# Optimization experiments

Measured on AMD Instinct MI355X. Metric: run time of the kernel, lower is better.

## Reference

```python
import jax, jax.numpy as jnp
import numpy as np

B, T, E = 64, 512, 128
NODES, PATHS, OUT = 100000, 200000, 1000
PAD = 1  # padding_idx for node embedding


def setup_inputs() -> dict:
    key = jax.random.key(0)
    ks = jax.random.split(key, 10)
    starts = jax.random.randint(ks[0], (B, T), 0, NODES)
    paths = jax.random.randint(ks[1], (B, T), 0, PATHS)
    ends = jax.random.randint(ks[2], (B, T), 0, NODES)
    length = jax.random.randint(ks[3], (B,), 0, T)
    node_emb = jax.random.normal(ks[4], (NODES, E), dtype=jnp.float32)
    path_emb = jax.random.normal(ks[5], (PATHS, E), dtype=jnp.float32)
    W = jax.random.normal(ks[6], (E, 3 * E), dtype=jnp.float32)
    a = jax.random.normal(ks[7], (E,), dtype=jnp.float32)
    out_W = jax.random.normal(ks[8], (OUT, E), dtype=jnp.float32) * (1.0 / np.sqrt(E))
    out_b = jax.random.normal(ks[9], (OUT,), dtype=jnp.float32) * 0.01
    return dict(starts=starts, paths=paths, ends=ends, length=length,
                node_emb=node_emb, path_emb=path_emb, W=W, a=a,
                out_W=out_W, out_b=out_b)


def reference(starts, paths, ends, length, node_emb, path_emb, W, a, out_W, out_b):
    # padding_idx=1 -> that embedding row is zero
    node_emb = node_emb.at[PAD].set(0.0)
    es = node_emb[starts]          # [B,T,E]
    ep = path_emb[paths]           # [B,T,E]
    ee = node_emb[ends]            # [B,T,E]
    c = jnp.concatenate([es, ep, ee], axis=2)          # [B,T,3E]
    # dropout is identity in eval mode
    x = jnp.tanh(jnp.einsum('ed,btd->bte', W, c))      # [B,T,E]
    z = jax.nn.softmax(x @ a, axis=1)                  # [B,T] softmax over full T
    # original code sums only first length[i] attention weights (no renorm)
    mask = (jnp.arange(T)[None, :] < length[:, None]).astype(x.dtype)  # [B,T]
    v = jnp.einsum('bte,bt->be', x, z * mask)          # [B,E]
    return v @ out_W.T + out_b                          # [B,OUT]
```

## Files before the change

### kernel.cpp

```cpp
#include <hip/hip_runtime.h>

#define BB     64
#define TT     512
#define EE     128
#define NROWS  (BB * TT)
#define PADIDX 1
#define OUTN   1000

typedef __attribute__((ext_vector_type(8)))  short short8;
typedef __attribute__((ext_vector_type(16))) float f32x16;

__device__ __forceinline__ float tanh_fast(float v) {
    return 1.0f - 2.0f / (__expf(2.0f * v) + 1.0f);
}

__device__ __forceinline__ unsigned short f2bf(float f) {
    unsigned int u = __float_as_uint(f);
    u += 0x7fffu + ((u >> 16) & 1u);
    return (unsigned short)(u >> 16);
}
__device__ __forceinline__ float bf2f(unsigned short h) {
    return __uint_as_float(((unsigned int)h) << 16);
}

__global__ __launch_bounds__(256, 1)
void k_gemm_x(const int* __restrict__ starts, const int* __restrict__ paths,
              const int* __restrict__ ends,
              const float* __restrict__ node_emb, const float* __restrict__ path_emb,
              const float* __restrict__ W, const float* __restrict__ a,
              float* __restrict__ x, float* __restrict__ s)
{
    __shared__ __align__(16) unsigned short Ah[128 * 64];
    __shared__ __align__(16) unsigned short Al[128 * 64];
    __shared__ __align__(16) unsigned short Wh[128 * 64];
    __shared__ __align__(16) unsigned short Wl[128 * 64];
    __shared__ int   idx_lds[3][128];
    __shared__ float s_red[128][2];

    const int tid = threadIdx.x;
    const int r0  = blockIdx.x * 128;

    if (tid < 128) {
        idx_lds[0][tid] = starts[r0 + tid];
        idx_lds[1][tid] = paths [r0 + tid];
        idx_lds[2][tid] = ends  [r0 + tid];
    }

    const int q    = tid & 15;
    const int ty   = tid >> 4;
    const int lane = tid & 63;
    const int wid  = tid >> 6;
    const int wm   = wid >> 1;
    const int wn   = wid & 1;
    const int fr   = lane & 31;
    const int fkb  = (lane >> 5) * 16;

    f32x16 acc[2][2];
#pragma unroll
    for (int mi = 0; mi < 2; ++mi)
#pragma unroll
        for (int ni = 0; ni < 2; ++ni)
#pragma unroll
            for (int i = 0; i < 16; ++i) acc[mi][ni][i] = 0.0f;

    float4 va[8], vw[8];

    __syncthreads();

#define LOAD_STAGE(T) do {                                                      \
    const int seg_ = (T) >> 1;                                                  \
    const int off_ = ((T) & 1) * 64;                                            \
    const float* emb_ = (seg_ == 1) ? path_emb : node_emb;                      \
    const bool isn_ = (seg_ != 1);                                              \
    _Pragma("unroll")                                                           \
    for (int it = 0; it < 8; ++it) {                                            \
        const int row_ = it * 16 + ty;                                          \
        const int idx_ = idx_lds[seg_][row_];                                   \
        va[it] = *((const float4*)(emb_ + (size_t)idx_ * EE + off_) + q);       \
        if (isn_ && idx_ == PADIDX) { va[it].x = 0.f; va[it].y = 0.f;           \
                                      va[it].z = 0.f; va[it].w = 0.f; }         \
        vw[it] = *((const float4*)(W + row_ * 384 + (T) * 64) + q);             \
    }                                                                           \
} while (0)

#define CVT_WRITE() do {                                                        \
    _Pragma("unroll")                                                           \
    for (int it = 0; it < 8; ++it) {                                            \
        const int row_  = it * 16 + ty;                                         \
        const int boff_ = row_ * 128 + ((q * 8) ^ ((row_ & 7) << 4));           \
        {                                                                       \
            const unsigned short h0 = f2bf(va[it].x), h1 = f2bf(va[it].y);      \
            const unsigned short h2 = f2bf(va[it].z), h3 = f2bf(va[it].w);      \
            uint2 hp; hp.x = (unsigned)h0 | ((unsigned)h1 << 16);               \
                      hp.y = (unsigned)h2 | ((unsigned)h3 << 16);               \
            *(uint2*)((char*)Ah + boff_) = hp;                                  \
            const unsigned short l0 = f2bf(va[it].x - bf2f(h0));                \
            const unsigned short l1 = f2bf(va[it].y - bf2f(h1));                \
            const unsigned short l2 = f2bf(va[it].z - bf2f(h2));                \
            const unsigned short l3 = f2bf(va[it].w - bf2f(h3));                \
            uint2 lp; lp.x = (unsigned)l0 | ((unsigned)l1 << 16);               \
                      lp.y = (unsigned)l2 | ((unsigned)l3 << 16);               \
            *(uint2*)((char*)Al + boff_) = lp;                                  \
        }                                                                       \
        {                                                                       \
            const unsigned short h0 = f2bf(vw[it].x), h1 = f2bf(vw[it].y);      \
            const unsigned short h2 = f2bf(vw[it].z), h3 = f2bf(vw[it].w);      \
            uint2 hp; hp.x = (unsigned)h0 | ((unsigned)h1 << 16);               \
                      hp.y = (unsigned)h2 | ((unsigned)h3 << 16);               \
            *(uint2*)((char*)Wh + boff_) = hp;                                  \
            const unsigned short l0 = f2bf(vw[it].x - bf2f(h0));                \
            const unsigned short l1 = f2bf(vw[it].y - bf2f(h1));                \
            const unsigned short l2 = f2bf(vw[it].z - bf2f(h2));                \
            const unsigned short l3 = f2bf(vw[it].w - bf2f(h3));                \
            uint2 lp; lp.x = (unsigned)l0 | ((unsigned)l1 << 16);               \
                      lp.y = (unsigned)l2 | ((unsigned)l3 << 16);               \
            *(uint2*)((char*)Wl + boff_) = lp;                                  \
        }                                                                       \
    }                                                                           \
} while (0)

#define COMPUTE() do {                                                          \
    _Pragma("unroll")                                                           \
    for (int ksub = 0; ksub < 4; ++ksub) {                                      \
        short8 ah[2], al2[2], bh[2], bl2[2];                                    \
        _Pragma("unroll")                                                       \
        for (int mi = 0; mi < 2; ++mi) {                                        \
            const int row_  = wm * 64 + mi * 32 + fr;                           \
            const int boff_ = row_ * 128 + ((ksub * 32 + fkb) ^ ((row_ & 7) << 4)); \
            ah[mi]  = *(const short8*)((const char*)Ah + boff_);                \
            al2[mi] = *(const short8*)((const char*)Al + boff_);                \
        }                                                                       \
        _Pragma("unroll")                                                       \
        for (int ni = 0; ni < 2; ++ni) {                                        \
            const int row_  = wn * 64 + ni * 32 + fr;                           \
            const int boff_ = row_ * 128 + ((ksub * 32 + fkb) ^ ((row_ & 7) << 4)); \
            bh[ni]  = *(const short8*)((const char*)Wh + boff_);                \
            bl2[ni] = *(const short8*)((const char*)Wl + boff_);                \
        }                                                                       \
        _Pragma("unroll")                                                       \
        for (int mi = 0; mi < 2; ++mi)                                          \
        _Pragma("unroll")                                                       \
        for (int ni = 0; ni < 2; ++ni) {                                        \
            acc[mi][ni] = __builtin_amdgcn_mfma_f32_32x32x16_bf16(ah[mi],  bh[ni],  acc[mi][ni], 0, 0, 0); \
            acc[mi][ni] = __builtin_amdgcn_mfma_f32_32x32x16_bf16(ah[mi],  bl2[ni], acc[mi][ni], 0, 0, 0); \
            acc[mi][ni] = __builtin_amdgcn_mfma_f32_32x32x16_bf16(al2[mi], bh[ni],  acc[mi][ni], 0, 0, 0); \
        }                                                                       \
    }                                                                           \
} while (0)

    LOAD_STAGE(0);
    CVT_WRITE();
    __syncthreads();

    for (int t = 0; t < 6; ++t) {
        if (t < 5) LOAD_STAGE(t + 1);
        COMPUTE();
        __syncthreads();
        if (t < 5) { CVT_WRITE(); __syncthreads(); }
    }

    const float a0 = a[wn * 64 + fr];
    const float a1 = a[wn * 64 + 32 + fr];
    const int hi_half = lane >> 5;

#pragma unroll
    for (int mi = 0; mi < 2; ++mi) {
        float sp[16];
#pragma unroll
        for (int r = 0; r < 16; ++r) sp[r] = 0.0f;
#pragma unroll
        for (int ni = 0; ni < 2; ++ni) {
            const float ac  = (ni == 0) ? a0 : a1;
            const int   col = wn * 64 + ni * 32 + fr;
#pragma unroll
            for (int r = 0; r < 16; ++r) {
                const int rowl = (r & 3) + 8 * (r >> 2) + 4 * hi_half;
                const float tv = tanh_fast(acc[mi][ni][r]);
                x[(size_t)(r0 + wm * 64 + mi * 32 + rowl) * EE + col] = tv;
                sp[r] = fmaf(tv, ac, sp[r]);
            }
        }
#pragma unroll
        for (int m = 1; m < 32; m <<= 1)
#pragma unroll
            for (int r = 0; r < 16; ++r) sp[r] += __shfl_xor(sp[r], m, 64);
        if (fr == 0) {
#pragma unroll
            for (int r = 0; r < 16; ++r) {
                const int rowl = (r & 3) + 8 * (r >> 2) + 4 * hi_half;
                s_red[wm * 64 + mi * 32 + rowl][wn] = sp[r];
            }
        }
    }
    __syncthreads();
    if (tid < 128) s[r0 + tid] = s_red[tid][0] + s_red[tid][1];
}

__global__ __launch_bounds__(256)
void k_attn(const float* __restrict__ s, const int* __restrict__ length,
            const float* __restrict__ x, float* __restrict__ v)
{
    __shared__ float sw[TT];
    __shared__ float red[256];

    const int b   = blockIdx.x >> 2;
    const int ec  = blockIdx.x & 3;
    const int tid = threadIdx.x;

    const float s0 = s[b * TT + tid];
    const float s1 = s[b * TT + 256 + tid];

    red[tid] = fmaxf(s0, s1);
    __syncthreads();
    for (int st = 128; st > 0; st >>= 1) {
        if (tid < st) red[tid] = fmaxf(red[tid], red[tid + st]);
        __syncthreads();
    }
    const float mx = red[0];
    __syncthreads();

    const float e0 = __expf(s0 - mx);
    const float e1 = __expf(s1 - mx);
    red[tid] = e0 + e1;
    __syncthreads();
    for (int st = 128; st > 0; st >>= 1) {
        if (tid < st) red[tid] += red[tid + st];
        __syncthreads();
    }
    const float inv = 1.0f / red[0];
    const int   len = length[b];
    __syncthreads();

    sw[tid]       = (tid < len)       ? e0 * inv : 0.0f;
    sw[tid + 256] = (tid + 256 < len) ? e1 * inv : 0.0f;
    __syncthreads();

    const int e  = ec * 32 + (tid & 31);
    const int tp = tid >> 5;
    const float* xb = x + (size_t)b * TT * EE;
    float acc = 0.0f;
#pragma unroll 8
    for (int t = tp; t < TT; t += 8)
        acc = fmaf(sw[t], xb[(size_t)t * EE + e], acc);

    red[tid] = acc;
    __syncthreads();
    if (tid < 32) {
        float r2 = 0.0f;
#pragma unroll
        for (int k = 0; k < 8; ++k) r2 += red[k * 32 + tid];
        v[b * EE + ec * 32 + tid] = r2;
    }
}

__global__ __launch_bounds__(256)
void k_out(const float* __restrict__ v, const float* __restrict__ out_W,
           const float* __restrict__ out_b, float* __restrict__ out)
{
    const int id = blockIdx.x * 256 + threadIdx.x;
    const int o  = id >> 6;
    const int bb = id & 63;

    const float4* vr = (const float4*)(v + bb * EE);
    const float4* wr = (const float4*)(out_W + o * EE);
    float acc = 0.0f;
#pragma unroll 8
    for (int qq = 0; qq < 32; ++qq) {
        const float4 a4 = vr[qq];
        const float4 b4 = wr[qq];
        acc = fmaf(a4.x, b4.x, acc);
        acc = fmaf(a4.y, b4.y, acc);
        acc = fmaf(a4.z, b4.z, acc);
        acc = fmaf(a4.w, b4.w, acc);
    }
    out[bb * OUTN + o] = acc + out_b[o];
}

extern "C" void kernel_launch(void* const* d_in, const int* in_sizes, int n_in,
                              void* d_out, int out_size, void* d_ws, size_t ws_size,
                              hipStream_t stream)
{
    const int*   starts   = (const int*)d_in[0];
    const int*   paths    = (const int*)d_in[1];
    const int*   ends     = (const int*)d_in[2];
    const int*   length   = (const int*)d_in[3];
    const float* node_emb = (const float*)d_in[4];
    const float* path_emb = (const float*)d_in[5];
    const float* W        = (const float*)d_in[6];
    const float* a        = (const float*)d_in[7];
    const float* out_W    = (const float*)d_in[8];
    const float* out_b    = (const float*)d_in[9];
    float*       out      = (float*)d_out;

    float* x = (float*)d_ws;
    float* s = x + (size_t)NROWS * EE;
    float* v = s + NROWS;

    k_gemm_x<<<NROWS / 128, 256, 0, stream>>>(starts, paths, ends,
                                              node_emb, path_emb, W, a, x, s);
    k_attn<<<BB * 4, 256, 0, stream>>>(s, length, x, v);
    k_out<<<(BB * OUTN) / 256, 256, 0, stream>>>(v, out_W, out_b, out);
}
```

Baseline: 221.0 us.

## Stream gathered rows into LDS asynchronously with double buffering and precomputed split W

Adds a prep kernel that splits W once into swizzled bf16 hi/lo tiles in workspace. The GEMM kernel now copies gathered embedding rows and the W tiles straight into double-buffered LDS with global_load_lds, using manual vmcnt waits so the next stage loads while the current one computes. The fp32-to-bf16 split of activations moves to register time inside compute. This removes per-stage register staging, conversion and extra barriers, but uses about 130KB of LDS, adds one more launch, and relies on hand-written waitcnt ordering.

```diff
diff --git a/kernel.cpp b/kernel.cpp
--- a/kernel.cpp
+++ b/kernel.cpp
@@ -1,4 +1,5 @@
 #include <hip/hip_runtime.h>
+#include <hip/hip_bf16.h>
 
 #define BB     64
 #define TT     512
@@ -14,46 +15,71 @@
     return 1.0f - 2.0f / (__expf(2.0f * v) + 1.0f);
 }
 
-__device__ __forceinline__ unsigned short f2bf(float f) {
-    unsigned int u = __float_as_uint(f);
-    u += 0x7fffu + ((u >> 16) & 1u);
-    return (unsigned short)(u >> 16);
-}
-__device__ __forceinline__ float bf2f(unsigned short h) {
-    return __uint_as_float(((unsigned int)h) << 16);
+__device__ __forceinline__ void split8(float4 a0, float4 a1, short8& hi, short8& lo) {
+    float f[8] = {a0.x, a0.y, a0.z, a0.w, a1.x, a1.y, a1.z, a1.w};
+#pragma unroll
+    for (int i = 0; i < 8; ++i) {
+        unsigned u = __float_as_uint(f[i]);
+        unsigned r = (u + (0x7fffu + ((u >> 16) & 1u))) & 0xffff0000u;
+        hi[i] = (short)(r >> 16);
+        lo[i] = (short)(__float_as_uint(f[i] - __uint_as_float(r)) >> 16);
+    }
+}
+
+__device__ __forceinline__ void gl_lds16(const void* g, void* l) {
+    __builtin_amdgcn_global_load_lds((const __attribute__((address_space(1))) void*)g,
+                                     (__attribute__((address_space(3))) void*)l, 16, 0, 0);
+}
+
+__global__ __launch_bounds__(256)
+void k_prep(const float* __restrict__ W, unsigned short* __restrict__ Whg,
+            unsigned short* __restrict__ Wlg)
+{
+    const int id = blockIdx.x * 256 + threadIdx.x;
+    const int e  = id & 127;
+    const int d  = id >> 7;
+    const float v = W[e * 384 + d];
+    const int t = d >> 6, k = d & 63;
+
+    unsigned u = __float_as_uint(v);
+    unsigned r = (u + (0x7fffu + ((u >> 16) & 1u))) & 0xffff0000u;
+    const unsigned short h = (unsigned short)(r >> 16);
+    const unsigned short l = (unsigned short)(__float_as_uint(v - __uint_as_float(r)) >> 16);
+
+    const int boff = t * 16384 + e * 128 + ((k * 2) ^ ((e & 7) << 4));
+    *(unsigned short*)((char*)Whg + boff) = h;
+    *(unsigned short*)((char*)Wlg + boff) = l;
 }
 
 __global__ __launch_bounds__(256, 1)
 void k_gemm_x(const int* __restrict__ starts, const int* __restrict__ paths,
               const int* __restrict__ ends,
               const float* __restrict__ node_emb, const float* __restrict__ path_emb,
-              const float* __restrict__ W, const float* __restrict__ a,
-              float* __restrict__ x, float* __restrict__ s)
-{
-    __shared__ __align__(16) unsigned short Ah[128 * 64];
-    __shared__ __align__(16) unsigned short Al[128 * 64];
-    __shared__ __align__(16) unsigned short Wh[128 * 64];
-    __shared__ __align__(16) unsigned short Wl[128 * 64];
-    __shared__ int   idx_lds[3][128];
-    __shared__ float s_red[128][2];
+              const unsigned short* __restrict__ Whg, const unsigned short* __restrict__ Wlg,
+              const float* __restrict__ a, float* __restrict__ x, float* __restrict__ s)
+{
+    extern __shared__ char smem[];
+    float*          Af      = (float*)smem;
+    unsigned short* Wh      = (unsigned short*)(smem + 65536);
+    unsigned short* Wl      = (unsigned short*)(smem + 98304);
+    int*            idx_lds = (int*)(smem + 131072);
+    float*          s_red   = (float*)(smem + 132608);
 
     const int tid = threadIdx.x;
     const int r0  = blockIdx.x * 128;
 
     if (tid < 128) {
-        idx_lds[0][tid] = starts[r0 + tid];
-        idx_lds[1][tid] = paths [r0 + tid];
-        idx_lds[2][tid] = ends  [r0 + tid];
-    }
-
-    const int q    = tid & 15;
-    const int ty   = tid >> 4;
+        idx_lds[0 * 128 + tid] = starts[r0 + tid];
+        idx_lds[1 * 128 + tid] = paths [r0 + tid];
+        idx_lds[2 * 128 + tid] = ends  [r0 + tid];
+    }
+
     const int lane = tid & 63;
-    const int wid  = tid >> 6;
-    const int wm   = wid >> 1;
-    const int wn   = wid & 1;
+    const int w    = tid >> 6;
+    const int wm   = w >> 1;
+    const int wn   = w & 1;
     const int fr   = lane & 31;
-    const int fkb  = (lane >> 5) * 16;
+    const int kh   = lane >> 5;
 
     f32x16 acc[2][2];
 #pragma unroll
@@ -63,105 +89,97 @@
 #pragma unroll
             for (int i = 0; i < 16; ++i) acc[mi][ni][i] = 0.0f;
 
-    float4 va[8], vw[8];
-
-    __syncthreads();
-
-#define LOAD_STAGE(T) do {                                                      \
-    const int seg_ = (T) >> 1;                                                  \
-    const int off_ = ((T) & 1) * 64;                                            \
-    const float* emb_ = (seg_ == 1) ? path_emb : node_emb;                      \
-    const bool isn_ = (seg_ != 1);                                              \
+    __syncthreads();
+
+    bool p0[2], p2[2];
+#pragma unroll
+    for (int mi = 0; mi < 2; ++mi) {
+        const int rm = wm * 64 + mi * 32 + fr;
+        p0[mi] = (idx_lds[0 * 128 + rm] == PADIDX);
+        p2[mi] = (idx_lds[2 * 128 + rm] == PADIDX);
+    }
+
+#define ISSUE(T) do {                                                           \
+    const int   seg_  = (T) >> 1;                                               \
+    const char* embc_ = (const char*)((seg_ == 1) ? path_emb : node_emb);       \
+    char*       afb_  = (char*)Af + (((T) & 1) ? 32768 : 0);                    \
     _Pragma("unroll")                                                           \
     for (int it = 0; it < 8; ++it) {                                            \
-        const int row_ = it * 16 + ty;                                          \
-        const int idx_ = idx_lds[seg_][row_];                                   \
-        va[it] = *((const float4*)(emb_ + (size_t)idx_ * EE + off_) + q);       \
-        if (isn_ && idx_ == PADIDX) { va[it].x = 0.f; va[it].y = 0.f;           \
-                                      va[it].z = 0.f; va[it].w = 0.f; }         \
-        vw[it] = *((const float4*)(W + row_ * 384 + (T) * 64) + q);             \
+        const int row_ = w * 32 + it * 4 + (lane >> 4);                         \
+        const int idx_ = idx_lds[seg_ * 128 + row_];                            \
+        const char* src_ = embc_ + (size_t)idx_ * 512 + ((T) & 1) * 256         \
+                         + (((lane & 15) * 16) ^ ((row_ & 7) << 4));            \
+        gl_lds16(src_, afb_ + (w * 32 + it * 4) * 256);                         \
+    }                                                                           \
+    char* whb_ = (char*)Wh + (((T) & 1) ? 16384 : 0);                           \
+    char* wlb_ = (char*)Wl + (((T) & 1) ? 16384 : 0);                           \
+    _Pragma("unroll")                                                           \
+    for (int rr = 0; rr < 4; ++rr) {                                            \
+        const int o_ = rr * 4096 + w * 1024;                                    \
+        gl_lds16((const char*)Whg + (T) * 16384 + o_ + lane * 16, whb_ + o_);   \
+        gl_lds16((const char*)Wlg + (T) * 16384 + o_ + lane * 16, wlb_ + o_);   \
     }                                                                           \
 } while (0)
 
-#define CVT_WRITE() do {                                                        \
-    _Pragma("unroll")                                                           \
-    for (int it = 0; it < 8; ++it) {                                            \
-        const int row_  = it * 16 + ty;                                         \
-        const int boff_ = row_ * 128 + ((q * 8) ^ ((row_ & 7) << 4));           \
-        {                                                                       \
-            const unsigned short h0 = f2bf(va[it].x), h1 = f2bf(va[it].y);      \
-            const unsigned short h2 = f2bf(va[it].z), h3 = f2bf(va[it].w);      \
-            uint2 hp; hp.x = (unsigned)h0 | ((unsigned)h1 << 16);               \
-                      hp.y = (unsigned)h2 | ((unsigned)h3 << 16);               \
-            *(uint2*)((char*)Ah + boff_) = hp;                                  \
-            const unsigned short l0 = f2bf(va[it].x - bf2f(h0));                \
-            const unsigned short l1 = f2bf(va[it].y - bf2f(h1));                \
-            const unsigned short l2 = f2bf(va[it].z - bf2f(h2));                \
-            const unsigned short l3 = f2bf(va[it].w - bf2f(h3));                \
-            uint2 lp; lp.x = (unsigned)l0 | ((unsigned)l1 << 16);               \
-                      lp.y = (unsigned)l2 | ((unsigned)l3 << 16);               \
-            *(uint2*)((char*)Al + boff_) = lp;                                  \
-        }                                                                       \
-        {                                                                       \
-            const unsigned short h0 = f2bf(vw[it].x), h1 = f2bf(vw[it].y);      \
-            const unsigned short h2 = f2bf(vw[it].z), h3 = f2bf(vw[it].w);      \
-            uint2 hp; hp.x = (unsigned)h0 | ((unsigned)h1 << 16);               \
-                      hp.y = (unsigned)h2 | ((unsigned)h3 << 16);               \
-            *(uint2*)((char*)Wh + boff_) = hp;                                  \
-            const unsigned short l0 = f2bf(vw[it].x - bf2f(h0));                \
-            const unsigned short l1 = f2bf(vw[it].y - bf2f(h1));                \
-            const unsigned short l2 = f2bf(vw[it].z - bf2f(h2));                \
-            const unsigned short l3 = f2bf(vw[it].w - bf2f(h3));                \
-            uint2 lp; lp.x = (unsigned)l0 | ((unsigned)l1 << 16);               \
-                      lp.y = (unsigned)l2 | ((unsigned)l3 << 16);               \
-            *(uint2*)((char*)Wl + boff_) = lp;                                  \
-        }                                                                       \
-    }                                                                           \
-} while (0)
-
-#define COMPUTE() do {                                                          \
+#define COMPUTE(T) do {                                                         \
+    const char* afc_ = (const char*)Af + (((T) & 1) ? 32768 : 0);               \
+    const char* whc_ = (const char*)Wh + (((T) & 1) ? 16384 : 0);               \
+    const char* wlc_ = (const char*)Wl + (((T) & 1) ? 16384 : 0);               \
     _Pragma("unroll")                                                           \
     for (int ksub = 0; ksub < 4; ++ksub) {                                      \
-        short8 ah[2], al2[2], bh[2], bl2[2];                                    \
+        short8 ah[2], al[2], bh[2], bl[2];                                      \
         _Pragma("unroll")                                                       \
         for (int mi = 0; mi < 2; ++mi) {                                        \
-            const int row_  = wm * 64 + mi * 32 + fr;                           \
-            const int boff_ = row_ * 128 + ((ksub * 32 + fkb) ^ ((row_ & 7) << 4)); \
-            ah[mi]  = *(const short8*)((const char*)Ah + boff_);                \
-            al2[mi] = *(const short8*)((const char*)Al + boff_);                \
+            const int row_ = wm * 64 + mi * 32 + fr;                            \
+            const int swz_ = (row_ & 7) << 4;                                   \
+            const int k0b_ = ksub * 64 + kh * 32;                               \
+            float4 a0 = *(const float4*)(afc_ + row_ * 256 + (k0b_ ^ swz_));    \
+            float4 a1 = *(const float4*)(afc_ + row_ * 256 + ((k0b_ + 16) ^ swz_)); \
+            const bool pad_ = ((T) < 2) ? p0[mi] : (((T) >= 4) ? p2[mi] : false); \
+            if (pad_) { a0 = make_float4(0.f, 0.f, 0.f, 0.f); a1 = a0; }        \
+            split8(a0, a1, ah[mi], al[mi]);                                     \
         }                                                                       \
         _Pragma("unroll")                                                       \
         for (int ni = 0; ni < 2; ++ni) {                                        \
-            const int row_  = wn * 64 + ni * 32 + fr;                           \
-            const int boff_ = row_ * 128 + ((ksub * 32 + fkb) ^ ((row_ & 7) << 4)); \
-            bh[ni]  = *(const short8*)((const char*)Wh + boff_);                \
-            bl2[ni] = *(const short8*)((const char*)Wl + boff_);                \
+            const int e_ = wn * 64 + ni * 32 + fr;                              \
+            const int bo_ = e_ * 128 + ((ksub * 32 + kh * 16) ^ ((e_ & 7) << 4)); \
+            bh[ni] = *(const short8*)(whc_ + bo_);                              \
+            bl[ni] = *(const short8*)(wlc_ + bo_);                              \
         }                                                                       \
         _Pragma("unroll")                                                       \
         for (int mi = 0; mi < 2; ++mi)                                          \
         _Pragma("unroll")                                                       \
         for (int ni = 0; ni < 2; ++ni) {                                        \
-            acc[mi][ni] = __builtin_amdgcn_mfma_f32_32x32x16_bf16(ah[mi],  bh[ni],  acc[mi][ni], 0, 0, 0); \
-            acc[mi][ni] = __builtin_amdgcn_mfma_f32_32x32x16_bf16(ah[mi],  bl2[ni], acc[mi][ni], 0, 0, 0); \
-            acc[mi][ni] = __builtin_amdgcn_mfma_f32_32x32x16_bf16(al2[mi], bh[ni],  acc[mi][ni], 0, 0, 0); \
+            acc[mi][ni] = __builtin_amdgcn_mfma_f32_32x32x16_bf16(ah[mi], bh[ni], acc[mi][ni], 0, 0, 0); \
+            acc[mi][ni] = __builtin_amdgcn_mfma_f32_32x32x16_bf16(ah[mi], bl[ni], acc[mi][ni], 0, 0, 0); \
+            acc[mi][ni] = __builtin_amdgcn_mfma_f32_32x32x16_bf16(al[mi], bh[ni], acc[mi][ni], 0, 0, 0); \
         }                                                                       \
     }                                                                           \
 } while (0)
 
-    LOAD_STAGE(0);
-    CVT_WRITE();
-    __syncthreads();
-
+    ISSUE(0);
+
+#pragma unroll
     for (int t = 0; t < 6; ++t) {
-        if (t < 5) LOAD_STAGE(t + 1);
-        COMPUTE();
-        __syncthreads();
-        if (t < 5) { CVT_WRITE(); __syncthreads(); }
-    }
-
-    const float a0 = a[wn * 64 + fr];
-    const float a1 = a[wn * 64 + 32 + fr];
-    const int hi_half = lane >> 5;
+        if (t < 5) {
+            ISSUE(t + 1);
+            asm volatile("s_waitcnt vmcnt(16)" ::: "memory");
+        } else {
+            asm volatile("s_waitcnt vmcnt(0)" ::: "memory");
+        }
+        __builtin_amdgcn_s_barrier();
+        __builtin_amdgcn_sched_barrier(0);
+        COMPUTE(t);
+        asm volatile("s_waitcnt lgkmcnt(0)" ::: "memory");
+        __builtin_amdgcn_sched_barrier(0);
+        __builtin_amdgcn_s_barrier();
+    }
+
+#undef ISSUE
+#undef COMPUTE
+
+    const float a0v = a[wn * 64 + fr];
+    const float a1v = a[wn * 64 + 32 + fr];
 
 #pragma unroll
     for (int mi = 0; mi < 2; ++mi) {
@@ -170,11 +188,11 @@
         for (int r = 0; r < 16; ++r) sp[r] = 0.0f;
 #pragma unroll
         for (int ni = 0; ni < 2; ++ni) {
-            const float ac  = (ni == 0) ? a0 : a1;
+            const float ac  = (ni == 0) ? a0v : a1v;
             const int   col = wn * 64 + ni * 32 + fr;
 #pragma unroll
             for (int r = 0; r < 16; ++r) {
-                const int rowl = (r & 3) + 8 * (r >> 2) + 4 * hi_half;
+                const int rowl = (r & 3) + 8 * (r >> 2) + 4 * kh;
                 const float tv = tanh_fast(acc[mi][ni][r]);
                 x[(size_t)(r0 + wm * 64 + mi * 32 + rowl) * EE + col] = tv;
                 sp[r] = fmaf(tv, ac, sp[r]);
@@ -187,13 +205,13 @@
         if (fr == 0) {
 #pragma unroll
             for (int r = 0; r < 16; ++r) {
-                const int rowl = (r & 3) + 8 * (r >> 2) + 4 * hi_half;
-                s_red[wm * 64 + mi * 32 + rowl][wn] = sp[r];
+                const int rowl = (r & 3) + 8 * (r >> 2) + 4 * kh;
+                s_red[(wm * 64 + mi * 32 + rowl) * 2 + wn] = sp[r];
             }
         }
     }
     __syncthreads();
-    if (tid < 128) s[r0 + tid] = s_red[tid][0] + s_red[tid][1];
+    if (tid < 128) s[r0 + tid] = s_red[tid * 2] + s_red[tid * 2 + 1];
 }
 
 __global__ __launch_bounds__(256)
@@ -295,9 +313,17 @@
     float* x = (float*)d_ws;
     float* s = x + (size_t)NROWS * EE;
     float* v = s + NROWS;
-
-    k_gemm_x<<<NROWS / 128, 256, 0, stream>>>(starts, paths, ends,
-                                              node_emb, path_emb, W, a, x, s);
+    unsigned short* Whg = (unsigned short*)(v + BB * EE);
+    unsigned short* Wlg = Whg + 6 * 8192;
+
+    static const int SMEM = 133632;
+    hipFuncSetAttribute((const void*)k_gemm_x,
+                        hipFuncAttributeMaxDynamicSharedMemorySize, SMEM);
+
+    k_prep<<<192, 256, 0, stream>>>(W, Whg, Wlg);
+    k_gemm_x<<<NROWS / 128, 256, SMEM, stream>>>(starts, paths, ends,
+                                                 node_emb, path_emb, Whg, Wlg,
+                                                 a, x, s);
     k_attn<<<BB * 4, 256, 0, stream>>>(s, length, x, v);
     k_out<<<(BB * OUTN) / 256, 256, 0, stream>>>(v, out_W, out_b, out);
 }
```

Result: faster. 209.0 us (-5.4%).
